# Optimization experiments

Measured on AMD Instinct MI355X. Metric: run time of the kernel, lower is better.

## Reference

```python
import jax, jax.numpy as jnp
import numpy as np

OUT = 16          # output_size
SCALE = 1.0 / 16.0  # 1/featmap_stride
GRID = 2          # sampling_ratio


def setup_inputs() -> dict:
    key = jax.random.key(0)
    k1, k2, k3 = jax.random.split(key, 3)
    N, C, T, H, W, K = 2, 256, 16, 56, 56, 5
    feat = jax.random.normal(k1, (N, C, T, H, W), jnp.float32)
    img = H * 16.0  # 896 px input image
    xy = jax.random.uniform(k2, (N, K, 2), minval=0.0, maxval=img - 300.0)
    wh = jax.random.uniform(k3, (N, K, 2), minval=32.0, maxval=290.0)
    boxes = jnp.concatenate([xy, xy + wh], axis=-1)  # valid xyxy boxes
    rois = jnp.concatenate([jnp.zeros((N, K, 1)), boxes], axis=-1).astype(jnp.float32)
    entity_mask = jnp.ones((N, 1, K, T), dtype=bool)  # unused by forward (as in original)
    return {"feat": feat, "rois": rois, "entity_mask": entity_mask}


def _roi_align_single(feat_n, boxes):
    """RoIAlign (aligned=True, avg pool, fixed sampling grid) for one clip.

    feat_n: (C, T, H, W) -- applied to every frame t at once.
    boxes:  (K, 4) xyxy in input-image coordinates.
    returns (T, K, C, OUT, OUT)
    """
    C, T, H, W = feat_n.shape
    K = boxes.shape[0]
    b = boxes * SCALE - 0.5  # aligned=True offset
    x1, y1, x2, y2 = b[:, 0], b[:, 1], b[:, 2], b[:, 3]
    bin_w = (x2 - x1) / OUT
    bin_h = (y2 - y1) / OUT
    g = (jnp.arange(GRID, dtype=feat_n.dtype) + 0.5) / GRID
    p = jnp.arange(OUT, dtype=feat_n.dtype)
    # sample coords per roi/bin/grid-point: (K, OUT, GRID)
    xs = x1[:, None, None] + (p[None, :, None] + g[None, None, :]) * bin_w[:, None, None]
    ys = y1[:, None, None] + (p[None, :, None] + g[None, None, :]) * bin_h[:, None, None]
    # full (K, OUT_h, OUT_w, GRID_h, GRID_w) coordinate grids
    Y = jnp.broadcast_to(ys[:, :, None, :, None], (K, OUT, OUT, GRID, GRID))
    X = jnp.broadcast_to(xs[:, None, :, None, :], (K, OUT, OUT, GRID, GRID))
    valid = (Y > -1.0) & (Y < H) & (X > -1.0) & (X < W)
    Yc = jnp.clip(Y, 0.0, H - 1.0)
    Xc = jnp.clip(X, 0.0, W - 1.0)
    y0 = jnp.floor(Yc).astype(jnp.int32)
    x0 = jnp.floor(Xc).astype(jnp.int32)
    y1i = jnp.minimum(y0 + 1, H - 1)
    x1i = jnp.minimum(x0 + 1, W - 1)
    ly = Yc - y0.astype(feat_n.dtype)
    lx = Xc - x0.astype(feat_n.dtype)
    hy = 1.0 - ly
    hx = 1.0 - lx
    m = valid.astype(feat_n.dtype)
    gat = lambda yi, xi: feat_n[:, :, yi, xi]  # -> (C, T, K, OUT, OUT, GRID, GRID)
    val = (gat(y0, x0) * (hy * hx * m)
           + gat(y0, x1i) * (hy * lx * m)
           + gat(y1i, x0) * (ly * hx * m)
           + gat(y1i, x1i) * (ly * lx * m))
    out = val.mean(axis=(-1, -2))  # avg over GRIDxGRID samples (mmcv divides by count)
    return out.transpose(1, 2, 0, 3, 4)  # (T, K, C, OUT, OUT)


def reference(feat, rois, entity_mask):
    # feat: (N, C, T, H, W); rois: (N, K, 5); entity_mask unused (as in original forward)
    boxes = rois[..., 1:5]
    roi_feats = jax.vmap(_roi_align_single)(feat, boxes)  # (N, T, K, C, OUT, OUT)
    return roi_feats, feat
```

## Files before the change

### kernel.cpp

```cpp
#include <hip/hip_runtime.h>

constexpr int N = 2, C = 256, T = 16, H = 56, W = 56, K = 5;
constexpr int CG = 4;
constexpr int ROI_TOTAL   = N * T * K * C * 16 * 16;
constexpr int FEAT_TOTAL  = N * C * T * H * W;
constexpr int ROI_BLOCKS  = N * T * K * (C / CG);

constexpr int COPY_V4_PER_BLOCK = 1024;
constexpr int COPY_BLOCKS = FEAT_TOTAL / 4 / COPY_V4_PER_BLOCK;

constexpr int CHUNK = 129, ROI_PER_CHUNK = 80, COPY_PER_CHUNK = 49;
constexpr int TOTAL_BLOCKS = COPY_BLOCKS + ROI_BLOCKS;

constexpr int WMAX = 22;
constexpr int LDSW = 23;
constexpr int WSZ  = WMAX * LDSW;
constexpr int NROW_UNROLL = 11;

typedef float floatx4 __attribute__((ext_vector_type(4)));

__global__ __launch_bounds__(256) void fused_roi_copy_kernel(
    const float* __restrict__ feat,
    const float* __restrict__ rois,
    float* __restrict__ roi_out,
    float* __restrict__ feat_out)
{
    __shared__ float win[CG * WSZ];
    __shared__ int   xoff[32], yoff[32];
    __shared__ float xh[32], xl[32], yh[32], yl[32];

    int chunk = blockIdx.x / CHUNK;
    int pos   = blockIdx.x - chunk * CHUNK;

    if (pos >= ROI_PER_CHUNK) {
        int cb   = chunk * COPY_PER_CHUNK + (pos - ROI_PER_CHUNK);
        int base = cb * COPY_V4_PER_BLOCK + threadIdx.x;
        const floatx4* src = (const floatx4*)feat;
        floatx4*       dst = (floatx4*)feat_out;
        floatx4 v0 = src[base];
        floatx4 v1 = src[base + 256];
        floatx4 v2 = src[base + 512];
        floatx4 v3 = src[base + 768];
        __builtin_nontemporal_store(v0, dst + base);
        __builtin_nontemporal_store(v1, dst + base + 256);
        __builtin_nontemporal_store(v2, dst + base + 512);
        __builtin_nontemporal_store(v3, dst + base + 768);
        return;
    }

    int rb   = chunk * ROI_PER_CHUNK + pos;
    int cg   = rb & 63;
    int rest = rb >> 6;
    int k  = rest % 5;
    int nt = rest / 5;
    int t  = nt & 15;
    int n  = nt >> 4;

    const float* r = rois + (n * K + k) * 5;
    float bx1 = r[1] * 0.0625f - 0.5f;
    float by1 = r[2] * 0.0625f - 0.5f;
    float bw  = (r[3] * 0.0625f - 0.5f - bx1) * 0.0625f;
    float bh  = (r[4] * 0.0625f - 0.5f - by1) * 0.0625f;

    float xmin = fminf(fmaxf(bx1 + 0.25f  * bw, 0.0f), (float)(W - 1));
    float xmax = fminf(fmaxf(bx1 + 15.75f * bw, 0.0f), (float)(W - 1));
    float ymin = fminf(fmaxf(by1 + 0.25f  * bh, 0.0f), (float)(H - 1));
    float ymax = fminf(fmaxf(by1 + 15.75f * bh, 0.0f), (float)(H - 1));
    int x_lo = (int)xmin, y_lo = (int)ymin;
    int ncx = min((int)xmax - x_lo + 2, WMAX);
    int ncy = min((int)ymax - y_lo + 2, WMAX);

    int tid = threadIdx.x;

    if (tid < 64) {
        int  i   = tid & 31;
        bool isY = tid >= 32;
        int  p   = i >> 1, g = i & 1;
        float b1  = isY ? by1 : bx1;
        float bs  = isY ? bh  : bw;
        float lim = (float)(isY ? H : W);
        int   lo  = isY ? y_lo : x_lo;
        float F  = b1 + ((float)p + (g ? 0.75f : 0.25f)) * bs;
        float m  = (F > -1.0f && F < lim) ? 1.0f : 0.0f;
        float Fc = fminf(fmaxf(F, 0.0f), lim - 1.0f);
        int   f0 = (int)Fc;
        float l  = Fc - (float)f0;
        float h  = 1.0f - l;
        if (isY) {
            yoff[i] = (f0 - lo) * LDSW;
            yh[i]   = h * m * 0.25f;
            yl[i]   = l * m * 0.25f;
        } else {
            xoff[i] = f0 - lo;
            xh[i]   = h * m;
            xl[i]   = l * m;
        }
    }

    {
        int lane = tid & 63;
        int wv   = __builtin_amdgcn_readfirstlane(tid >> 6);
        int col  = lane & 31;
        int r0   = lane >> 5;
        const float* fp = feat
            + (size_t)(((n * C + (cg * CG + wv)) * T) + t) * (H * W);
        float* wb = win + wv * WSZ;
        int  xg    = min(x_lo + col, W - 1);
        bool colok = col < ncx;

        float v[NROW_UNROLL];
        #pragma unroll
        for (int u = 0; u < NROW_UNROLL; ++u) {
            int rr = r0 + 2 * u;
            int y  = min(y_lo + min(rr, ncy - 1), H - 1);
            v[u] = fp[y * W + xg];
        }
        #pragma unroll
        for (int u = 0; u < NROW_UNROLL; ++u) {
            int rr = r0 + 2 * u;
            if (colok && rr < ncy)
                wb[rr * LDSW + col] = v[u];
        }
    }
    __syncthreads();

    int px = tid & 15;
    int py = tid >> 4;

    int   xo0 = xoff[2 * px],     xo1 = xoff[2 * px + 1];
    float hx0 = xh[2 * px],       lx0 = xl[2 * px];
    float hx1 = xh[2 * px + 1],   lx1 = xl[2 * px + 1];
    int   yo0 = yoff[2 * py],     yo1 = yoff[2 * py + 1];
    float hy0 = yh[2 * py],       ly0 = yl[2 * py];
    float hy1 = yh[2 * py + 1],   ly1 = yl[2 * py + 1];

    int i00 = yo0 + xo0, i01 = yo0 + xo1;
    int i10 = yo1 + xo0, i11 = yo1 + xo1;

#define SAMP(idx, HY, LY, HX, LX)                                         \
    ((HY) * ((HX) * wbc[(idx)] + (LX) * wbc[(idx) + 1]) +                 \
     (LY) * ((HX) * wbc[(idx) + LDSW] + (LX) * wbc[(idx) + LDSW + 1]))

    int obase = (rest * C + cg * CG) * 256 + tid;
#pragma unroll
    for (int cc = 0; cc < CG; ++cc) {
        const float* wbc = win + cc * WSZ;
        float acc = SAMP(i00, hy0, ly0, hx0, lx0)
                  + SAMP(i01, hy0, ly0, hx1, lx1)
                  + SAMP(i10, hy1, ly1, hx0, lx0)
                  + SAMP(i11, hy1, ly1, hx1, lx1);
        __builtin_nontemporal_store(acc, roi_out + obase + cc * 256);
    }
#undef SAMP
}

extern "C" void kernel_launch(void* const* d_in, const int* in_sizes, int n_in,
                              void* d_out, int out_size, void* d_ws, size_t ws_size,
                              hipStream_t stream)
{
    const float* feat = (const float*)d_in[0];
    const float* rois = (const float*)d_in[1];

    float* roi_out  = (float*)d_out;
    float* feat_out = (float*)d_out + ROI_TOTAL;

    fused_roi_copy_kernel<<<TOTAL_BLOCKS, 256, 0, stream>>>(
        feat, rois, roi_out, feat_out);
}
```

Baseline: 223.3 us.

## Split fused ROI/copy kernel into separate copy and ROIAlign launches

Replaces the single interleaved kernel, which mixed copy blocks and ROI blocks in fixed chunks, with two sequential launches: a plain feature-copy kernel moving 8 float4 per thread, then the ROIAlign kernel. The nontemporal stores in both paths become ordinary stores. The change drops the per-block chunk dispatch arithmetic and lets the second kernel read feat while it may still be cache-resident from the copy. The cost is a second launch and the loss of overlap between the bandwidth-bound copy and the ROI computation.

```diff
diff --git a/kernel.cpp b/kernel.cpp
--- a/kernel.cpp
+++ b/kernel.cpp
@@ -1,54 +1,41 @@
 #include <hip/hip_runtime.h>
 
 constexpr int N = 2, C = 256, T = 16, H = 56, W = 56, K = 5;
-constexpr int CG = 4;
-constexpr int ROI_TOTAL   = N * T * K * C * 16 * 16;
-constexpr int FEAT_TOTAL  = N * C * T * H * W;
-constexpr int ROI_BLOCKS  = N * T * K * (C / CG);
+constexpr int ROI_TOTAL  = N * T * K * C * 16 * 16;
+constexpr int FEAT_TOTAL = N * C * T * H * W;
+constexpr int ROI_BLOCKS = N * T * K * (C / 4);
 
-constexpr int COPY_V4_PER_BLOCK = 1024;
-constexpr int COPY_BLOCKS = FEAT_TOTAL / 4 / COPY_V4_PER_BLOCK;
-
-constexpr int CHUNK = 129, ROI_PER_CHUNK = 80, COPY_PER_CHUNK = 49;
-constexpr int TOTAL_BLOCKS = COPY_BLOCKS + ROI_BLOCKS;
+constexpr int COPY_BLOCKS = 3136;
 
 constexpr int WMAX = 22;
 constexpr int LDSW = 23;
 constexpr int WSZ  = WMAX * LDSW;
+constexpr int CG   = 4;
 constexpr int NROW_UNROLL = 11;
 
 typedef float floatx4 __attribute__((ext_vector_type(4)));
 
-__global__ __launch_bounds__(256) void fused_roi_copy_kernel(
+__global__ __launch_bounds__(256) void copy_kernel(
+    const float* __restrict__ feat, float* __restrict__ feat_out)
+{
+    const floatx4* src = (const floatx4*)feat;
+    floatx4*       dst = (floatx4*)feat_out;
+    int base = blockIdx.x * 2048 + threadIdx.x;
+    #pragma unroll
+    for (int u = 0; u < 8; ++u)
+        dst[base + u * 256] = src[base + u * 256];
+}
+
+__global__ __launch_bounds__(256) void roi_kernel(
     const float* __restrict__ feat,
     const float* __restrict__ rois,
-    float* __restrict__ roi_out,
-    float* __restrict__ feat_out)
+    float* __restrict__ roi_out)
 {
     __shared__ float win[CG * WSZ];
     __shared__ int   xoff[32], yoff[32];
     __shared__ float xh[32], xl[32], yh[32], yl[32];
 
-    int chunk = blockIdx.x / CHUNK;
-    int pos   = blockIdx.x - chunk * CHUNK;
-
-    if (pos >= ROI_PER_CHUNK) {
-        int cb   = chunk * COPY_PER_CHUNK + (pos - ROI_PER_CHUNK);
-        int base = cb * COPY_V4_PER_BLOCK + threadIdx.x;
-        const floatx4* src = (const floatx4*)feat;
-        floatx4*       dst = (floatx4*)feat_out;
-        floatx4 v0 = src[base];
-        floatx4 v1 = src[base + 256];
-        floatx4 v2 = src[base + 512];
-        floatx4 v3 = src[base + 768];
-        __builtin_nontemporal_store(v0, dst + base);
-        __builtin_nontemporal_store(v1, dst + base + 256);
-        __builtin_nontemporal_store(v2, dst + base + 512);
-        __builtin_nontemporal_store(v3, dst + base + 768);
-        return;
-    }
-
-    int rb   = chunk * ROI_PER_CHUNK + pos;
+    int rb   = blockIdx.x;
     int cg   = rb & 63;
     int rest = rb >> 6;
     int k  = rest % 5;
@@ -149,7 +136,7 @@
                   + SAMP(i01, hy0, ly0, hx1, lx1)
                   + SAMP(i10, hy1, ly1, hx0, lx0)
                   + SAMP(i11, hy1, ly1, hx1, lx1);
-        __builtin_nontemporal_store(acc, roi_out + obase + cc * 256);
+        roi_out[obase + cc * 256] = acc;
     }
 #undef SAMP
 }
@@ -164,6 +151,6 @@
     float* roi_out  = (float*)d_out;
     float* feat_out = (float*)d_out + ROI_TOTAL;
 
-    fused_roi_copy_kernel<<<TOTAL_BLOCKS, 256, 0, stream>>>(
-        feat, rois, roi_out, feat_out);
+    copy_kernel<<<COPY_BLOCKS, 256, 0, stream>>>(feat, feat_out);
+    roi_kernel<<<ROI_BLOCKS, 256, 0, stream>>>(feat, rois, roi_out);
 }
```

Measured after the change: 239.9 us. 7.4% more time.
